# Performance work log

Measured on AMD Instinct MI355X. Metric: run time of the kernel, lower is better.

The kernel has to match this reference:

```python
import jax, jax.numpy as jnp
import numpy as np

B, S, H, D = 2, 2048, 2048, 256  # batch, seq, hidden, head_dim
NH, NKV = 8, 1                   # attention heads, kv heads
N_REP = NH // NKV
SCALING = D ** -0.5
ROPE_THETA = 10000.0
NEG_INF = -1e9


def rotate_half(x):
    x1, x2 = jnp.split(x, 2, axis=-1)
    return jnp.concatenate((-x2, x1), axis=-1)


def setup_inputs() -> dict:
    key = jax.random.key(0)
    ks = jax.random.split(key, 5)
    hidden_states = jax.random.normal(ks[0], (B, S, H), dtype=jnp.float32)
    # RoPE cos/sin per position, Gemma-style: inv_freq tiled over full head_dim
    inv_freq = 1.0 / (ROPE_THETA ** (np.arange(0, D, 2, dtype=np.float32) / D))  # [D/2]
    pos = np.arange(S, dtype=np.float32)
    freqs = np.outer(pos, inv_freq)                      # [S, D/2]
    emb = np.concatenate([freqs, freqs], axis=-1)        # [S, D]
    cos = jnp.broadcast_to(jnp.asarray(np.cos(emb)), (B, S, D))
    sin = jnp.broadcast_to(jnp.asarray(np.sin(emb)), (B, S, D))
    # additive causal mask [B, 1, S, S]
    causal = jnp.triu(jnp.full((S, S), NEG_INF, dtype=jnp.float32), k=1)
    attention_mask = jnp.broadcast_to(causal[None, None], (B, 1, S, S))
    scale = 0.02
    Wq = jax.random.normal(ks[1], (H, NH * D), dtype=jnp.float32) * scale
    Wk = jax.random.normal(ks[2], (H, NKV * D), dtype=jnp.float32) * scale
    Wv = jax.random.normal(ks[3], (H, NKV * D), dtype=jnp.float32) * scale
    Wo = jax.random.normal(ks[4], (NH * D, H), dtype=jnp.float32) * scale
    return {"hidden_states": hidden_states, "cos": cos, "sin": sin,
            "attention_mask": attention_mask, "Wq": Wq, "Wk": Wk, "Wv": Wv, "Wo": Wo}


def reference(hidden_states, cos, sin, attention_mask, Wq, Wk, Wv, Wo):
    # projections: [B,S,H] @ [H, nh*D] -> [B, nh, S, D]
    q = (hidden_states @ Wq).reshape(B, S, NH, D).transpose(0, 2, 1, 3)
    k = (hidden_states @ Wk).reshape(B, S, NKV, D).transpose(0, 2, 1, 3)
    v = (hidden_states @ Wv).reshape(B, S, NKV, D).transpose(0, 2, 1, 3)
    # RoPE (cos/sin broadcast over head dim via unsqueeze at axis 1)
    c = cos[:, None]  # [B,1,S,D]
    s = sin[:, None]
    q = q * c + rotate_half(q) * s
    k = k * c + rotate_half(k) * s
    # repeat_kv: [B, NKV, S, D] -> [B, NH, S, D]
    k = jnp.repeat(k, N_REP, axis=1)
    v = jnp.repeat(v, N_REP, axis=1)
    # eager attention
    attn_weights = jnp.einsum("bhqd,bhkd->bhqk", q, k) * SCALING
    attn_weights = attn_weights + attention_mask[:, :, :, :S]
    attn_weights = jax.nn.softmax(attn_weights.astype(jnp.float32), axis=-1).astype(q.dtype)
    attn_output = jnp.einsum("bhqk,bhkd->bhqd", attn_weights, v)
    attn_output = attn_output.transpose(0, 2, 1, 3).reshape(B, S, NH * D)
    attn_output = attn_output @ Wo
    return attn_output, attn_weights
```

## Files before the change

kernel.cpp:

```cpp
#include <hip/hip_runtime.h>
#include <hip/hip_bf16.h>

#define B_   2
#define S_   2048
#define H_   2048
#define D_   256
#define NH_  8

typedef unsigned short u16;
typedef __bf16 bf16x8 __attribute__((ext_vector_type(8)));
typedef float f32x4 __attribute__((ext_vector_type(4)));
typedef unsigned int uint4v __attribute__((ext_vector_type(4)));
typedef unsigned int uint2v __attribute__((ext_vector_type(2)));

#define AS1 __attribute__((address_space(1)))
#define AS3 __attribute__((address_space(3)))

__device__ __forceinline__ u16 f2bf(float x) {
  union { float f; unsigned u; } v; v.f = x;
  unsigned u = v.u;
  u += 0x7FFFu + ((u >> 16) & 1u);
  return (u16)(u >> 16);
}
__device__ __forceinline__ float bf2f(u16 x) {
  union { unsigned u; float f; } v; v.u = ((unsigned)x) << 16;
  return v.f;
}

__device__ __forceinline__ void gld_lds16(const u16* g, u16* l) {
  __builtin_amdgcn_global_load_lds((const AS1 unsigned int*)g,
                                   (AS3 unsigned int*)l, 16, 0, 0);
}

#define BM 128
#define BN 128
#define BK 32

enum GemmMode { MODE_PROJ = 0, MODE_QK = 1, MODE_PV = 2, MODE_WO = 3 };

template <int MODE>
__global__ __launch_bounds__(256)
void gemm_nt(const u16* __restrict__ A, const u16* __restrict__ Bb,
             void* __restrict__ Cp, float* __restrict__ rows,
             float* __restrict__ Pout,
             int K, int lda, int ldb, int ldc)
{
  int bn, bm;
  if constexpr (MODE == MODE_QK) {
    int t = blockIdx.x;
    bm = 0;
    while ((bm + 1) * (bm + 2) / 2 <= t) bm++;
    bn = t - bm * (bm + 1) / 2;
  } else if constexpr (MODE == MODE_PV) {
    bn = blockIdx.x;
    bm = (int)gridDim.y - 1 - (int)blockIdx.y;
  } else {
    bn = blockIdx.x;
    bm = blockIdx.y;
  }
  const int bz = blockIdx.z;
  const int m0 = bm * BM, n0 = bn * BN;

  const u16* Ap = A;
  const u16* Bp = Bb;
  float* Cf = (float*)Cp;
  u16*   Cu = (u16*)Cp;
  float* Pp = Pout;

  if constexpr (MODE == MODE_QK) {
    Ap   += (size_t)bz * S_ * D_;
    Bp   += (size_t)(bz >> 3) * S_ * D_;
    Cu   += (size_t)bz * S_ * S_;
    rows += (size_t)bz * S_;
  } else if constexpr (MODE == MODE_PV) {
    Ap   += (size_t)bz * S_ * S_;
    Bp   += (size_t)(bz >> 3) * D_ * S_;
    Cu   += (size_t)(bz >> 3) * S_ * (NH_ * D_) + (size_t)(bz & 7) * D_;
    rows += (size_t)bz * S_;
    Pp   += (size_t)bz * S_ * S_;
  }

  int Keff = K;
  if constexpr (MODE == MODE_PV) {
    int lim = (bm + 1) * BM;
    Keff = lim < K ? lim : K;
  }

  __shared__ __align__(16) u16 smem[BM * BK + BN * BK + 512];
  u16* As = smem;
  u16* Bs = smem + BM * BK;
  __shared__ float invs[BM];

  const int tid  = threadIdx.x;
  const int lane = tid & 63;
  const int quad = lane >> 4;
  const int l16  = lane & 15;
  const int wave = tid >> 6;
  const int wm   = (wave >> 1) << 6;
  const int wn   = (wave & 1) << 6;

  if constexpr (MODE == MODE_PV) {
    if (tid < BM) invs[tid] = 1.0f / rows[m0 + tid];
  }

  f32x4 acc[4][4] = {};

  for (int kt = 0; kt < Keff; kt += BK) {
    #pragma unroll
    for (int i = 0; i < 2; i++) {
      int c = tid + i * 256;
      gld_lds16(Ap + (size_t)(m0 + (c >> 2)) * lda + kt + (c & 3) * 8, &As[c * 8]);
    }
    #pragma unroll
    for (int i = 0; i < 2; i++) {
      int c = tid + i * 256;
      gld_lds16(Bp + (size_t)(n0 + (c >> 2)) * ldb + kt + (c & 3) * 8, &Bs[c * 8]);
    }
    __syncthreads();

    bf16x8 af[4], bfr[4];
    #pragma unroll
    for (int i = 0; i < 4; i++)
      af[i] = *(const bf16x8*)(&As[(wm + i * 16 + l16) * BK + quad * 8]);
    #pragma unroll
    for (int j = 0; j < 4; j++)
      bfr[j] = *(const bf16x8*)(&Bs[(wn + j * 16 + l16) * BK + quad * 8]);
    #pragma unroll
    for (int i = 0; i < 4; i++)
      #pragma unroll
      for (int j = 0; j < 4; j++)
        acc[i][j] = __builtin_amdgcn_mfma_f32_16x16x32_bf16(af[i], bfr[j], acc[i][j], 0, 0, 0);

    if constexpr (MODE == MODE_PV) {
      if (bn == 0) {
        const int r8 = tid >> 3;
        const int c8 = tid & 7;
        #pragma unroll
        for (int rr = 0; rr < BM; rr += 32) {
          const int r = rr + r8;
          const u16* e = &As[r * BK + c8 * 4];
          const float inv = invs[r];
          float4 o;
          o.x = bf2f(e[0]) * inv; o.y = bf2f(e[1]) * inv;
          o.z = bf2f(e[2]) * inv; o.w = bf2f(e[3]) * inv;
          *(float4*)(Pp + (size_t)(m0 + r) * S_ + kt + c8 * 4) = o;
        }
      }
    }
    __syncthreads();
  }

  if constexpr (MODE == MODE_PV) {
    if (bn == 0 && Keff < S_) {
      const int r8 = tid >> 3;
      const int c8 = tid & 7;
      const float4 z = {0.f, 0.f, 0.f, 0.f};
      #pragma unroll
      for (int rr = 0; rr < BM; rr += 32) {
        float* pr = Pp + (size_t)(m0 + rr + r8) * S_;
        for (int c4 = (Keff >> 2) + c8; c4 < (S_ >> 2); c4 += 8)
          *(float4*)(pr + c4 * 4) = z;
      }
    }
  }

  const float SCL2 = 0.0625f * 1.44269504088896340736f;
  if constexpr (MODE == MODE_WO) {
    float (*Cs32)[132] = (float (*)[132])smem;
    const int band16 = (wave >> 1) * 16;
    #pragma unroll
    for (int i = 0; i < 4; i++) {
      #pragma unroll
      for (int r = 0; r < 4; r++) {
        const int lr = band16 + quad * 4 + r;
        #pragma unroll
        for (int j = 0; j < 4; j++)
          Cs32[lr][wn + j * 16 + l16] = acc[i][j][r];
      }
      __syncthreads();
      #pragma unroll
      for (int ch = tid; ch < 1024; ch += 256) {
        const int rr = ch >> 5, cc = ch & 31;
        const int mg = m0 + ((rr >> 4) << 6) + i * 16 + (rr & 15);
        *(float4*)(Cf + (size_t)mg * ldc + n0 + cc * 4) =
            *(const float4*)(&Cs32[rr][cc * 4]);
      }
      __syncthreads();
    }
  } else {
    u16 (*Cs)[136] = (u16 (*)[136])smem;
    const int band16 = (wave >> 1) * 16;
    #pragma unroll
    for (int i = 0; i < 4; i++) {
      #pragma unroll
      for (int r = 0; r < 4; r++) {
        const int lr = band16 + quad * 4 + r;
        const int m  = m0 + wm + i * 16 + quad * 4 + r;
        if constexpr (MODE == MODE_QK) {
          float rs = 0.f;
          #pragma unroll
          for (int j = 0; j < 4; j++) {
            int n = n0 + wn + j * 16 + l16;
            float e = (n <= m) ? exp2f(acc[i][j][r] * SCL2) : 0.f;
            rs += e;
            Cs[lr][wn + j * 16 + l16] = f2bf(e);
          }
          #pragma unroll
          for (int o = 1; o < 16; o <<= 1) rs += __shfl_xor(rs, o, 64);
          if (l16 == 0) atomicAdd(&rows[m], rs);
        } else if constexpr (MODE == MODE_PV) {
          const float inv = invs[wm + i * 16 + quad * 4 + r];
          #pragma unroll
          for (int j = 0; j < 4; j++)
            Cs[lr][wn + j * 16 + l16] = f2bf(acc[i][j][r] * inv);
        } else {
          #pragma unroll
          for (int j = 0; j < 4; j++)
            Cs[lr][wn + j * 16 + l16] = f2bf(acc[i][j][r]);
        }
      }
      __syncthreads();
      #pragma unroll
      for (int ch = tid; ch < 512; ch += 256) {
        const int rr = ch >> 4, cc = ch & 15;
        const int mg = m0 + ((rr >> 4) << 6) + i * 16 + (rr & 15);
        *(uint4v*)(Cu + (size_t)mg * ldc + n0 + cc * 8) =
            *(const uint4v*)(&Cs[rr][cc * 8]);
      }
      __syncthreads();
    }
  }
}

__device__ __forceinline__ void tc_tile(const float* __restrict__ src,
                                        u16* __restrict__ dst, int K, int N,
                                        int n0, int k0, float (*t)[33])
{
  int c = threadIdx.x & 31, r = threadIdx.x >> 5;
  #pragma unroll
  for (int rr = 0; rr < 32; rr += 8)
    t[r + rr][c] = src[(size_t)(k0 + r + rr) * N + n0 + c];
  __syncthreads();
  #pragma unroll
  for (int rr = 0; rr < 32; rr += 8)
    dst[(size_t)(n0 + r + rr) * K + k0 + c] = f2bf(t[c][r + rr]);
}

__global__ __launch_bounds__(256)
void prep_kernel(const float* __restrict__ X,
                 const float* __restrict__ Wq, const float* __restrict__ Wk,
                 const float* __restrict__ Wv, const float* __restrict__ Wo,
                 u16* __restrict__ Xbf, u16* __restrict__ WT,
                 u16* __restrict__ WoT)
{
  __shared__ float t[32][33];
  const int bid = blockIdx.x;
  if (bid < 4096) {
    tc_tile(Wq, WT, 2048, 2048, (bid & 63) * 32, (bid >> 6) * 32, t);
  } else if (bid < 4608) {
    int l = bid - 4096;
    tc_tile(Wk, WT + 2048 * 2048, 2048, 256, (l & 7) * 32, (l >> 3) * 32, t);
  } else if (bid < 5120) {
    int l = bid - 4608;
    tc_tile(Wv, WT + 2304 * 2048, 2048, 256, (l & 7) * 32, (l >> 3) * 32, t);
  } else if (bid < 9216) {
    int l = bid - 5120;
    tc_tile(Wo, WoT, 2048, 2048, (l & 63) * 32, (l >> 6) * 32, t);
  } else {
    int l = bid - 9216;
    #pragma unroll
    for (int it = 0; it < 4; ++it) {
      int i = it * 524288 + l * 256 + threadIdx.x;
      float4 f = ((const float4*)X)[i];
      uint2v p;
      p.x = (unsigned)f2bf(f.x) | ((unsigned)f2bf(f.y) << 16);
      p.y = (unsigned)f2bf(f.z) | ((unsigned)f2bf(f.w) << 16);
      ((uint2v*)Xbf)[i] = p;
    }
  }
}

__global__ __launch_bounds__(256)
void postproj_kernel(const u16* __restrict__ raw, const float* __restrict__ cosb,
                     const float* __restrict__ sinb, u16* __restrict__ qout,
                     u16* __restrict__ kout, u16* __restrict__ vt)
{
  __shared__ u16 t[32][34];
  const int bid = blockIdx.x;
  if (bid < 1024) {
    const int d    = threadIdx.x & 127;
    const int half = threadIdx.x >> 7;
    #pragma unroll
    for (int it = 0; it < 16; ++it) {
      int idx = bid * 32 + it * 2 + half;
      int h = idx & 7, bs = idx >> 3;
      int b = bs >> 11, s = bs & (S_ - 1);
      size_t base = (size_t)bs * 2560 + (size_t)h * D_;
      float q1 = bf2f(raw[base + d]);
      float q2 = bf2f(raw[base + 128 + d]);
      float c  = cosb[(size_t)bs * D_ + d];
      float sn = sinb[(size_t)bs * D_ + d];
      size_t ob = (((size_t)b * NH_ + h) * S_ + s) * D_;
      qout[ob + d]       = f2bf(q1 * c - q2 * sn);
      qout[ob + 128 + d] = f2bf(q2 * c + q1 * sn);
    }
  } else if (bid < 1280) {
    const int l    = bid - 1024;
    const int d    = threadIdx.x & 127;
    const int half = threadIdx.x >> 7;
    #pragma unroll
    for (int it = 0; it < 8; ++it) {
      int bs = l * 16 + it * 2 + half;
      size_t base = (size_t)bs * 2560 + 2048;
      float k1 = bf2f(raw[base + d]);
      float k2 = bf2f(raw[base + 128 + d]);
      float c  = cosb[(size_t)bs * D_ + d];
      float sn = sinb[(size_t)bs * D_ + d];
      kout[(size_t)bs * D_ + d]       = f2bf(k1 * c - k2 * sn);
      kout[(size_t)bs * D_ + 128 + d] = f2bf(k2 * c + k1 * sn);
    }
  } else {
    int l = bid - 1280;
    int b = l >> 9, rem = l & 511;
    int d0 = (rem & 7) * 32, s0 = (rem >> 3) * 32;
    int c = threadIdx.x & 31, r = threadIdx.x >> 5;
    #pragma unroll
    for (int rr = 0; rr < 32; rr += 8)
      t[r + rr][c] = raw[(size_t)(b * S_ + s0 + r + rr) * 2560 + 2304 + d0 + c];
    __syncthreads();
    #pragma unroll
    for (int rr = 0; rr < 32; rr += 8)
      vt[(size_t)b * D_ * S_ + (size_t)(d0 + r + rr) * S_ + s0 + c] = t[c][r + rr];
  }
}

extern "C" void kernel_launch(void* const* d_in, const int* in_sizes, int n_in,
                              void* d_out, int out_size, void* d_ws, size_t ws_size,
                              hipStream_t stream)
{
  const float* X    = (const float*)d_in[0];
  const float* cosb = (const float*)d_in[1];
  const float* sinb = (const float*)d_in[2];
  const float* Wq   = (const float*)d_in[4];
  const float* Wk   = (const float*)d_in[5];
  const float* Wv   = (const float*)d_in[6];
  const float* Wo   = (const float*)d_in[7];

  float* outO = (float*)d_out;
  float* outP = outO + (size_t)B_ * S_ * H_;

  u16* ws     = (u16*)d_ws;
  u16* Xbf    = ws;
  u16* WT     = Xbf    + 8388608;
  u16* WoT    = WT     + 5242880;
  u16* QKVraw = WoT    + 4194304;
  u16* Qbf    = QKVraw + 10485760;
  u16* Kbf    = Qbf    + 8388608;
  u16* VT     = Kbf    + 1048576;
  u16* AObf   = VT     + 1048576;
  u16* Ebf    = AObf   + 8388608;
  float* Rows = (float*)(Ebf + 67108864);

  prep_kernel<<<11264, 256, 0, stream>>>(X, Wq, Wk, Wv, Wo, Xbf, WT, WoT);
  gemm_nt<MODE_PROJ><<<dim3(20, 32, 1), 256, 0, stream>>>(
      Xbf, WT, QKVraw, nullptr, nullptr, 2048, 2048, 2048, 2560);
  postproj_kernel<<<2304, 256, 0, stream>>>(QKVraw, cosb, sinb, Qbf, Kbf, VT);
  hipMemsetAsync(Rows, 0, 32768 * sizeof(float), stream);
  gemm_nt<MODE_QK><<<dim3(136, 1, 16), 256, 0, stream>>>(
      Qbf, Kbf, Ebf, Rows, nullptr, 256, 256, 256, 2048);
  gemm_nt<MODE_PV><<<dim3(2, 16, 16), 256, 0, stream>>>(
      Ebf, VT, AObf, Rows, outP, 2048, 2048, 2048, 2048);
  gemm_nt<MODE_WO><<<dim3(16, 32, 1), 256, 0, stream>>>(
      AObf, WoT, outO, nullptr, nullptr, 2048, 2048, 2048, 2048);
}
```

Measured before the change: 638.5 us.

## Split softmax-probability writeout into dedicated PV blocks and vectorize RoPE

Moves the normalized attention-weight writeout (fp32 P matrix, 268MB) out of the bn==0 PV GEMM blocks into a third set of dedicated blocks that stream E rows with 16-byte loads and write full rows, including the zeroed masked region. This removes the serialization where half of the PV blocks did both MFMA work and the large store. It also vectorizes the RoPE post-projection kernel to 8-element loads and stores, and folds the Rows memset into the prep kernel to drop a separate launch. The new writeout blocks run 128 sequential rows each, which may limit parallelism.

```diff
diff --git a/kernel.cpp b/kernel.cpp
--- a/kernel.cpp
+++ b/kernel.cpp
@@ -25,6 +25,21 @@
 __device__ __forceinline__ float bf2f(u16 x) {
   union { unsigned u; float f; } v; v.u = ((unsigned)x) << 16;
   return v.f;
+}
+
+__device__ __forceinline__ void bf8_unpack(uint4v u, float* f) {
+  f[0] = bf2f(u.x & 0xffff); f[1] = bf2f(u.x >> 16);
+  f[2] = bf2f(u.y & 0xffff); f[3] = bf2f(u.y >> 16);
+  f[4] = bf2f(u.z & 0xffff); f[5] = bf2f(u.z >> 16);
+  f[6] = bf2f(u.w & 0xffff); f[7] = bf2f(u.w >> 16);
+}
+__device__ __forceinline__ uint4v bf8_pack(const float* f) {
+  uint4v o;
+  o.x = (unsigned)f2bf(f[0]) | ((unsigned)f2bf(f[1]) << 16);
+  o.y = (unsigned)f2bf(f[2]) | ((unsigned)f2bf(f[3]) << 16);
+  o.z = (unsigned)f2bf(f[4]) | ((unsigned)f2bf(f[5]) << 16);
+  o.w = (unsigned)f2bf(f[6]) | ((unsigned)f2bf(f[7]) << 16);
+  return o;
 }
 
 __device__ __forceinline__ void gld_lds16(const u16* g, u16* l) {
@@ -60,6 +75,7 @@
   }
   const int bz = blockIdx.z;
   const int m0 = bm * BM, n0 = bn * BN;
+  const int tid = threadIdx.x;
 
   const u16* Ap = A;
   const u16* Bp = Bb;
@@ -80,6 +96,35 @@
     Pp   += (size_t)bz * S_ * S_;
   }
 
+  if constexpr (MODE == MODE_PV) {
+    if (bn == 2) {
+      const int k0 = tid * 8;
+      for (int rr = 0; rr < BM; ++rr) {
+        const int q = m0 + rr;
+        const u16* e = Ap + (size_t)q * S_ + k0;
+        float* p = Pp + (size_t)q * S_ + k0;
+        const float inv = 1.0f / rows[q];
+        float4 lo = {0.f, 0.f, 0.f, 0.f}, hi = {0.f, 0.f, 0.f, 0.f};
+        if (k0 <= q) {
+          uint4v u = *(const uint4v*)e;
+          float v[8];
+          bf8_unpack(u, v);
+          lo.x = (k0 + 0 <= q) ? v[0] * inv : 0.f;
+          lo.y = (k0 + 1 <= q) ? v[1] * inv : 0.f;
+          lo.z = (k0 + 2 <= q) ? v[2] * inv : 0.f;
+          lo.w = (k0 + 3 <= q) ? v[3] * inv : 0.f;
+          hi.x = (k0 + 4 <= q) ? v[4] * inv : 0.f;
+          hi.y = (k0 + 5 <= q) ? v[5] * inv : 0.f;
+          hi.z = (k0 + 6 <= q) ? v[6] * inv : 0.f;
+          hi.w = (k0 + 7 <= q) ? v[7] * inv : 0.f;
+        }
+        *(float4*)p       = lo;
+        *(float4*)(p + 4) = hi;
+      }
+      return;
+    }
+  }
+
   int Keff = K;
   if constexpr (MODE == MODE_PV) {
     int lim = (bm + 1) * BM;
@@ -91,7 +136,6 @@
   u16* Bs = smem + BM * BK;
   __shared__ float invs[BM];
 
-  const int tid  = threadIdx.x;
   const int lane = tid & 63;
   const int quad = lane >> 4;
   const int l16  = lane & 15;
@@ -130,38 +174,7 @@
       #pragma unroll
       for (int j = 0; j < 4; j++)
         acc[i][j] = __builtin_amdgcn_mfma_f32_16x16x32_bf16(af[i], bfr[j], acc[i][j], 0, 0, 0);
-
-    if constexpr (MODE == MODE_PV) {
-      if (bn == 0) {
-        const int r8 = tid >> 3;
-        const int c8 = tid & 7;
-        #pragma unroll
-        for (int rr = 0; rr < BM; rr += 32) {
-          const int r = rr + r8;
-          const u16* e = &As[r * BK + c8 * 4];
-          const float inv = invs[r];
-          float4 o;
-          o.x = bf2f(e[0]) * inv; o.y = bf2f(e[1]) * inv;
-          o.z = bf2f(e[2]) * inv; o.w = bf2f(e[3]) * inv;
-          *(float4*)(Pp + (size_t)(m0 + r) * S_ + kt + c8 * 4) = o;
-        }
-      }
-    }
     __syncthreads();
-  }
-
-  if constexpr (MODE == MODE_PV) {
-    if (bn == 0 && Keff < S_) {
-      const int r8 = tid >> 3;
-      const int c8 = tid & 7;
-      const float4 z = {0.f, 0.f, 0.f, 0.f};
-      #pragma unroll
-      for (int rr = 0; rr < BM; rr += 32) {
-        float* pr = Pp + (size_t)(m0 + rr + r8) * S_;
-        for (int c4 = (Keff >> 2) + c8; c4 < (S_ >> 2); c4 += 8)
-          *(float4*)(pr + c4 * 4) = z;
-      }
-    }
   }
 
   const float SCL2 = 0.0625f * 1.44269504088896340736f;
@@ -251,7 +264,7 @@
                  const float* __restrict__ Wq, const float* __restrict__ Wk,
                  const float* __restrict__ Wv, const float* __restrict__ Wo,
                  u16* __restrict__ Xbf, u16* __restrict__ WT,
-                 u16* __restrict__ WoT)
+                 u16* __restrict__ WoT, float* __restrict__ Rows)
 {
   __shared__ float t[32][33];
   const int bid = blockIdx.x;
@@ -266,7 +279,7 @@
   } else if (bid < 9216) {
     int l = bid - 5120;
     tc_tile(Wo, WoT, 2048, 2048, (l & 63) * 32, (l >> 6) * 32, t);
-  } else {
+  } else if (bid < 11264) {
     int l = bid - 9216;
     #pragma unroll
     for (int it = 0; it < 4; ++it) {
@@ -277,6 +290,12 @@
       p.y = (unsigned)f2bf(f.z) | ((unsigned)f2bf(f.w) << 16);
       ((uint2v*)Xbf)[i] = p;
     }
+  } else {
+    int l = bid - 11264;
+    const float4 z = {0.f, 0.f, 0.f, 0.f};
+    #pragma unroll
+    for (int it = 0; it < 4; ++it)
+      ((float4*)Rows)[it * 2048 + l * 256 + threadIdx.x] = z;
   }
 }
 
@@ -288,37 +307,60 @@
   __shared__ u16 t[32][34];
   const int bid = blockIdx.x;
   if (bid < 1024) {
-    const int d    = threadIdx.x & 127;
-    const int half = threadIdx.x >> 7;
-    #pragma unroll
-    for (int it = 0; it < 16; ++it) {
-      int idx = bid * 32 + it * 2 + half;
+    const int row = threadIdx.x >> 4;
+    const int d8  = (threadIdx.x & 15) * 8;
+    #pragma unroll
+    for (int it2 = 0; it2 < 2; ++it2) {
+      int idx = bid * 32 + it2 * 16 + row;
       int h = idx & 7, bs = idx >> 3;
       int b = bs >> 11, s = bs & (S_ - 1);
       size_t base = (size_t)bs * 2560 + (size_t)h * D_;
-      float q1 = bf2f(raw[base + d]);
-      float q2 = bf2f(raw[base + 128 + d]);
-      float c  = cosb[(size_t)bs * D_ + d];
-      float sn = sinb[(size_t)bs * D_ + d];
+      uint4v u1 = *(const uint4v*)(raw + base + d8);
+      uint4v u2 = *(const uint4v*)(raw + base + 128 + d8);
+      float4 c0 = *(const float4*)(cosb + (size_t)bs * D_ + d8);
+      float4 c1 = *(const float4*)(cosb + (size_t)bs * D_ + d8 + 4);
+      float4 s0 = *(const float4*)(sinb + (size_t)bs * D_ + d8);
+      float4 s1 = *(const float4*)(sinb + (size_t)bs * D_ + d8 + 4);
+      float a[8], bq[8], cc[8], ss[8], r1[8], r2[8];
+      bf8_unpack(u1, a); bf8_unpack(u2, bq);
+      cc[0]=c0.x; cc[1]=c0.y; cc[2]=c0.z; cc[3]=c0.w;
+      cc[4]=c1.x; cc[5]=c1.y; cc[6]=c1.z; cc[7]=c1.w;
+      ss[0]=s0.x; ss[1]=s0.y; ss[2]=s0.z; ss[3]=s0.w;
+      ss[4]=s1.x; ss[5]=s1.y; ss[6]=s1.z; ss[7]=s1.w;
+      #pragma unroll
+      for (int i = 0; i < 8; ++i) {
+        r1[i] = a[i] * cc[i] - bq[i] * ss[i];
+        r2[i] = bq[i] * cc[i] + a[i] * ss[i];
+      }
       size_t ob = (((size_t)b * NH_ + h) * S_ + s) * D_;
-      qout[ob + d]       = f2bf(q1 * c - q2 * sn);
-      qout[ob + 128 + d] = f2bf(q2 * c + q1 * sn);
+      *(uint4v*)(qout + ob + d8)       = bf8_pack(r1);
+      *(uint4v*)(qout + ob + 128 + d8) = bf8_pack(r2);
     }
   } else if (bid < 1280) {
-    const int l    = bid - 1024;
-    const int d    = threadIdx.x & 127;
-    const int half = threadIdx.x >> 7;
-    #pragma unroll
-    for (int it = 0; it < 8; ++it) {
-      int bs = l * 16 + it * 2 + half;
-      size_t base = (size_t)bs * 2560 + 2048;
-      float k1 = bf2f(raw[base + d]);
-      float k2 = bf2f(raw[base + 128 + d]);
-      float c  = cosb[(size_t)bs * D_ + d];
-      float sn = sinb[(size_t)bs * D_ + d];
-      kout[(size_t)bs * D_ + d]       = f2bf(k1 * c - k2 * sn);
-      kout[(size_t)bs * D_ + 128 + d] = f2bf(k2 * c + k1 * sn);
-    }
+    const int l   = bid - 1024;
+    const int row = threadIdx.x >> 4;
+    const int d8  = (threadIdx.x & 15) * 8;
+    int bs = l * 16 + row;
+    size_t base = (size_t)bs * 2560 + 2048;
+    uint4v u1 = *(const uint4v*)(raw + base + d8);
+    uint4v u2 = *(const uint4v*)(raw + base + 128 + d8);
+    float4 c0 = *(const float4*)(cosb + (size_t)bs * D_ + d8);
+    float4 c1 = *(const float4*)(cosb + (size_t)bs * D_ + d8 + 4);
+    float4 s0 = *(const float4*)(sinb + (size_t)bs * D_ + d8);
+    float4 s1 = *(const float4*)(sinb + (size_t)bs * D_ + d8 + 4);
+    float a[8], bq[8], cc[8], ss[8], r1[8], r2[8];
+    bf8_unpack(u1, a); bf8_unpack(u2, bq);
+    cc[0]=c0.x; cc[1]=c0.y; cc[2]=c0.z; cc[3]=c0.w;
+    cc[4]=c1.x; cc[5]=c1.y; cc[6]=c1.z; cc[7]=c1.w;
+    ss[0]=s0.x; ss[1]=s0.y; ss[2]=s0.z; ss[3]=s0.w;
+    ss[4]=s1.x; ss[5]=s1.y; ss[6]=s1.z; ss[7]=s1.w;
+    #pragma unroll
+    for (int i = 0; i < 8; ++i) {
+      r1[i] = a[i] * cc[i] - bq[i] * ss[i];
+      r2[i] = bq[i] * cc[i] + a[i] * ss[i];
+    }
+    *(uint4v*)(kout + (size_t)bs * D_ + d8)       = bf8_pack(r1);
+    *(uint4v*)(kout + (size_t)bs * D_ + 128 + d8) = bf8_pack(r2);
   } else {
     int l = bid - 1280;
     int b = l >> 9, rem = l & 511;
@@ -361,14 +403,13 @@
   u16* Ebf    = AObf   + 8388608;
   float* Rows = (float*)(Ebf + 67108864);
 
-  prep_kernel<<<11264, 256, 0, stream>>>(X, Wq, Wk, Wv, Wo, Xbf, WT, WoT);
+  prep_kernel<<<11272, 256, 0, stream>>>(X, Wq, Wk, Wv, Wo, Xbf, WT, WoT, Rows);
   gemm_nt<MODE_PROJ><<<dim3(20, 32, 1), 256, 0, stream>>>(
       Xbf, WT, QKVraw, nullptr, nullptr, 2048, 2048, 2048, 2560);
   postproj_kernel<<<2304, 256, 0, stream>>>(QKVraw, cosb, sinb, Qbf, Kbf, VT);
-  hipMemsetAsync(Rows, 0, 32768 * sizeof(float), stream);
   gemm_nt<MODE_QK><<<dim3(136, 1, 16), 256, 0, stream>>>(
       Qbf, Kbf, Ebf, Rows, nullptr, 256, 256, 256, 2048);
-  gemm_nt<MODE_PV><<<dim3(2, 16, 16), 256, 0, stream>>>(
+  gemm_nt<MODE_PV><<<dim3(3, 16, 16), 256, 0, stream>>>(
       Ebf, VT, AObf, Rows, outP, 2048, 2048, 2048, 2048);
   gemm_nt<MODE_WO><<<dim3(16, 32, 1), 256, 0, stream>>>(
       AObf, WoT, outO, nullptr, nullptr, 2048, 2048, 2048, 2048);
```

Measured after the change: 662.7 us. +3.8%, slower.
